# Performance work log

Measured on AMD Instinct MI355X. Metric: run time of the kernel, lower is better.

Reference implementation:

```python
import jax, jax.numpy as jnp
import numpy as np

EPS = 1e-5  # torch BatchNorm default eps
B, C, T, NOUT, NCLS = 4096, 32, 512, 16, 4


def setup_inputs() -> dict:
    key = jax.random.key(0)
    ks = jax.random.split(key, 12)
    s = lambda k, shape: jax.random.normal(k, shape, jnp.float32) * 0.05
    return {
        "de": jax.random.normal(ks[0], (B, C, T), jnp.float32),
        "adj": jax.random.normal(ks[1], (B, C, C), jnp.float32),  # unused by forward (module recomputes corr)
        "dw_w": s(ks[2], (C, 1, 3)),      # depthwise Conv1d weight [C,1,3]
        "dw_b": s(ks[3], (C,)),
        "pw_w": s(ks[4], (C, C)),          # pointwise 1x1 conv [out,in]
        "pw_b": s(ks[5], (C,)),
        "bn1_g": jnp.ones((C,), jnp.float32),
        "bn1_b": jnp.zeros((C,), jnp.float32),
        "gc_w": s(ks[6], (T, NOUT)),       # GraphConvolution weight
        "fc_w": s(ks[7], (C * NOUT, C)),   # fc62 Linear(512,32)
        "fc_b": s(ks[8], (C,)),
        "bn2_g": jnp.ones((C,), jnp.float32),
        "bn2_b": jnp.zeros((C,), jnp.float32),
        "cls_w": s(ks[9], (C, NCLS)),      # fcclass Linear(32,4)
        "cls_b": s(ks[10], (NCLS,)),
    }


def reference(de, adj, dw_w, dw_b, pw_w, pw_b, bn1_g, bn1_b, gc_w,
              fc_w, fc_b, bn2_g, bn2_b, cls_w, cls_b):
    # --- SeparableConv2d (really 1d): depthwise k=3 -> pointwise 1x1 -> BN -> relu ---
    x = jax.lax.conv_general_dilated(
        de, dw_w, window_strides=(1,), padding=[(1, 1)],
        dimension_numbers=("NCH", "OIH", "NCH"),
        feature_group_count=de.shape[1]) + dw_b[None, :, None]
    x = jnp.einsum("oc,bct->bot", pw_w, x) + pw_b[None, :, None]
    m = x.mean((0, 2), keepdims=True)
    v = x.var((0, 2), keepdims=True)  # biased, as BN normalization uses
    x = (x - m) / jnp.sqrt(v + EPS) * bn1_g[None, :, None] + bn1_b[None, :, None]
    x = jax.nn.relu(x)                       # [B, C, T]

    # --- batched Pearson corrcoef over the time axis (vectorizes the per-sample loop) ---
    xt = x.transpose(0, 2, 1)                # [B, T, C]
    Tn = xt.shape[1]
    f = (Tn - 1) / Tn
    xc = xt - xt.mean(1, keepdims=True)
    num = jnp.einsum("btn,btm->bnm", xc, xc) / Tn   # biased covariance
    var = xt.var(1, ddof=1)                         # torch var default unbiased
    den = jnp.sqrt(var[:, :, None] * var[:, None, :]) * f
    cor = num / den                          # [B, C, C]

    # --- Chebyshev graph convolution (single K term, adj = cor) + relu ---
    g = jnp.einsum("bnm,bmt->bnt", cor, x)   # message passing over channel graph
    g = jax.nn.relu(jnp.einsum("bnt,to->bno", g, gc_w))  # [B, C, 16]

    # --- fc62: Linear -> BN1d -> (dropout: identity) -> sigmoid ---
    h = g.reshape(g.shape[0], -1) @ fc_w + fc_b          # [B, 32]
    m2 = h.mean(0)
    v2 = h.var(0)
    h = (h - m2) / jnp.sqrt(v2 + EPS) * bn2_g + bn2_b
    h = jax.nn.sigmoid(h)

    return h @ cls_w + cls_b                 # [B, 4]
```

## Files before the change

### kernel.cpp

```cpp
#include <hip/hip_runtime.h>
#include <math.h>

#define BB 4096
#define CC 32
#define TT 512
#define NOUTC 16
#define EPSF 1e-5f
#define XS 520


typedef __attribute__((ext_vector_type(16))) float f32x16;
typedef __attribute__((ext_vector_type(4)))  float f32x4;
typedef __attribute__((ext_vector_type(8)))  short short8;
typedef __attribute__((ext_vector_type(8)))  _Float16 half8;
typedef __attribute__((ext_vector_type(4)))  unsigned int u32x4;
typedef __attribute__((ext_vector_type(2)))  unsigned int u32x2;
typedef __attribute__((ext_vector_type(2)))  float vf2;
typedef __attribute__((ext_vector_type(4)))  float vf4;
typedef vf4 __attribute__((aligned(4))) vf4u;
typedef vf2 __attribute__((aligned(4))) vf2u;

__device__ __forceinline__ unsigned short f2b(float f) {
  unsigned int u = __builtin_bit_cast(unsigned int, f);
  return (unsigned short)((u + 0x7FFFu + ((u >> 16) & 1u)) >> 16);
}
__device__ __forceinline__ float blo(unsigned int u) {
  return __builtin_bit_cast(float, u << 16);
}
__device__ __forceinline__ float bhi(unsigned int u) {
  return __builtin_bit_cast(float, u & 0xFFFF0000u);
}
__device__ __forceinline__ unsigned int pk2(float a, float b) {
  return (unsigned int)f2b(a) | ((unsigned int)f2b(b) << 16);
}
__device__ __forceinline__ unsigned short h16(float f) {
  _Float16 h = (_Float16)f;
  return __builtin_bit_cast(unsigned short, h);
}
__device__ __forceinline__ unsigned int h2pk(float a, float b) {
  return (unsigned int)h16(a) | ((unsigned int)h16(b) << 16);
}

__device__ __forceinline__ void conv_cols(const float* __restrict__ deb,
    const float* __restrict__ dw, const float* __restrict__ db_,
    int tid, float* x1A, float* x1B) {
  int t0 = tid * 2;
  int off = (tid == 0) ? 0 : ((tid == 255) ? t0 - 2 : t0 - 1);
#pragma unroll
  for (int c = 0; c < CC; c++) {
    vf4u v = *reinterpret_cast<const vf4u*>(deb + c * TT + off);
    float vm1 = (tid == 0) ? 0.f : ((tid == 255) ? v.y : v.x);
    float v0  = (tid == 0) ? v.x : ((tid == 255) ? v.z : v.y);
    float vp1 = (tid == 0) ? v.y : ((tid == 255) ? v.w : v.z);
    float vp2 = (tid == 0) ? v.z : ((tid == 255) ? 0.f : v.w);
    float w0 = dw[c * 3], w1 = dw[c * 3 + 1], w2 = dw[c * 3 + 2], bc = db_[c];
    x1A[c] = fmaf(w0, vm1, fmaf(w1, v0, fmaf(w2, vp1, bc)));
    x1B[c] = fmaf(w0, v0, fmaf(w1, vp1, fmaf(w2, vp2, bc)));
  }
}

__global__ __launch_bounds__(256, 4) void k1_stats(const float* __restrict__ de,
    const float* __restrict__ dw, const float* __restrict__ db_,
    const float* __restrict__ pw, const float* __restrict__ pwb,
    const float* __restrict__ gcw,
    float* __restrict__ wsv, unsigned short* __restrict__ gcf,
    unsigned int* __restrict__ x2h, int useWs) {
  __shared__ __align__(16) unsigned short ldsX[13392];
  __shared__ float pbe_s[CC];
  __shared__ float sqb[4][64];
  const int XFo = 0, A3o = 10320;

  int tid = threadIdx.x, b = blockIdx.x;
  int lane = tid & 63, w = tid >> 6;
  int m31 = lane & 31, kh = lane >> 5;
  int p = tid >> 7, rp = tid & 127;

  if (b == 0) {
    for (int i = tid; i < TT * NOUTC; i += 256) {
      int e = i & 7, ln = (i >> 3) & 63, j = (i >> 9) & 7, w2 = i >> 12;
      int q = ln >> 4, n16 = ln & 15;
      int t = w2 * 256 + q * 8 + j * 32 + e;
      gcf[i] = f2b(gcw[t * 16 + n16]);
    }
  }

  for (int i = tid; i < 3 * CC * CC; i += 256) {
    int k = i >> 10, rem = i & 1023, o = rem >> 5, c = rem & 31;
    ldsX[A3o + i] = h16(pw[o * CC + c] * dw[c * 3 + k]);
  }
  if (tid < CC) {
    float s = pwb[tid];
#pragma unroll
    for (int c = 0; c < CC; c++) s = fmaf(pw[tid * CC + c], db_[c], s);
    pbe_s[tid] = s;
  }

  const float* deb = de + (size_t)b * CC * TT;
  unsigned int* xw = x2h + (size_t)b * (CC * 256);

  float sA[16], qA[16];
#pragma unroll
  for (int r = 0; r < 16; r++) { sA[r] = 0.f; qA[r] = 0.f; }
  float pbv[16];

#pragma unroll
  for (int h = 0; h < 2; h++) {
    if (h > 0) __syncthreads();
    {
      int t0 = h * 256 + 2 * rp - 1;
      int r0 = 2 * rp;
      int tl = (t0 < 0) ? 0 : t0;
#pragma unroll
      for (int cc = 0; cc < 16; cc += 2) {
        int c = 16 * p + cc;
        vf2 va = *(const vf2u*)(deb + c * TT + tl);
        vf2 vb = *(const vf2u*)(deb + (c + 1) * TT + tl);
        if (t0 < 0) { va.y = va.x; va.x = 0.f; vb.y = vb.x; vb.x = 0.f; }
        *(unsigned int*)&ldsX[XFo + r0 * 40 + c] = h2pk(va.x, vb.x);
        *(unsigned int*)&ldsX[XFo + (r0 + 1) * 40 + c] = h2pk(va.y, vb.y);
      }
      if (rp >= 126) {
        int r2 = 256 + (rp - 126);
        int t2 = h * 256 + r2 - 1;
#pragma unroll
        for (int cc = 0; cc < 16; cc++) {
          int c = 16 * p + cc;
          float v = (t2 < TT) ? deb[c * TT + t2] : 0.f;
          ldsX[XFo + r2 * 40 + c] = h16(v);
        }
      }
    }
    __syncthreads();
    if (h == 0) {
#pragma unroll
      for (int r = 0; r < 16; r++) pbv[r] = pbe_s[(r & 3) + 8 * (r >> 2) + 4 * kh];
    }
#pragma unroll
    for (int i = 0; i < 2; i++) {
      int wt = w * 2 + i;
      f32x16 acc;
#pragma unroll
      for (int r = 0; r < 16; r++) acc[r] = 0.f;
      int rowb = wt * 32 + m31;
#pragma unroll
      for (int k = 0; k < 3; k++) {
#pragma unroll
        for (int s = 0; s < 2; s++) {
          half8 af = *(const half8*)&ldsX[A3o + k * 1024 + m31 * 32 + s * 16 + kh * 8];
          half8 bf = *(const half8*)&ldsX[XFo + (rowb + k) * 40 + s * 16 + kh * 8];
          acc = __builtin_amdgcn_mfma_f32_32x32x16_f16(af, bf, acc, 0, 0, 0);
        }
      }
#pragma unroll
      for (int q4 = 0; q4 < 4; q4++) {
        float v0 = acc[4 * q4 + 0] + pbv[4 * q4 + 0];
        float v1 = acc[4 * q4 + 1] + pbv[4 * q4 + 1];
        float v2 = acc[4 * q4 + 2] + pbv[4 * q4 + 2];
        float v3 = acc[4 * q4 + 3] + pbv[4 * q4 + 3];
        sA[4 * q4 + 0] += v0; qA[4 * q4 + 0] = fmaf(v0, v0, qA[4 * q4 + 0]);
        sA[4 * q4 + 1] += v1; qA[4 * q4 + 1] = fmaf(v1, v1, qA[4 * q4 + 1]);
        sA[4 * q4 + 2] += v2; qA[4 * q4 + 2] = fmaf(v2, v2, qA[4 * q4 + 2]);
        sA[4 * q4 + 3] += v3; qA[4 * q4 + 3] = fmaf(v3, v3, qA[4 * q4 + 3]);
        if (useWs) {
          u32x2 pr2;
          pr2[0] = pk2(v0, v1);
          pr2[1] = pk2(v2, v3);
          *(u32x2*)(xw + ((((size_t)h * 8 + wt) * 4 + q4) * 2 + kh) * 64 + m31 * 2) = pr2;
        }
      }
    }
  }

#pragma unroll
  for (int r = 0; r < 16; r++) {
    float s = sA[r], q = qA[r];
#pragma unroll
    for (int d = 1; d < 32; d <<= 1) { s += __shfl_xor(s, d); q += __shfl_xor(q, d); }
    sA[r] = s; qA[r] = q;
  }
  if (m31 == 0) {
#pragma unroll
    for (int r = 0; r < 16; r++) {
      int o = (r & 3) + 8 * (r >> 2) + 4 * kh;
      sqb[w][o * 2 + 0] = sA[r];
      sqb[w][o * 2 + 1] = qA[r];
    }
  }
  __syncthreads();
  if (tid < 64) {
    int o = tid >> 1, st = tid & 1;
    float v = sqb[0][tid] + sqb[1][tid] + sqb[2][tid] + sqb[3][tid];
    atomicAdd(&wsv[st * 32 + o], v);
  }
}

__global__ __launch_bounds__(256, 3) void k3_main(const float* __restrict__ de,
    const float* __restrict__ dw, const float* __restrict__ db_,
    const float* __restrict__ pw, const float* __restrict__ pwb,
    const float* __restrict__ wsv, const float* __restrict__ bn1g,
    const float* __restrict__ bn1b, const unsigned short* __restrict__ gcf,
    const float* __restrict__ fcw, const float* __restrict__ fcb,
    float* __restrict__ hT, const unsigned int* __restrict__ x2h, int useWs) {
  __shared__ __align__(16) unsigned short x_s[CC * XS];
  __shared__ float gramP[2][CC * CC];
  __shared__ float zP[2][CC * NOUTC];
  __shared__ float red16[CC * 8];
  __shared__ float mu_s[CC], inv_s[CC];
  __shared__ float scsh[64];

  int tid = threadIdx.x, b = blockIdx.x;
  int w = tid >> 6, lane = tid & 63;
  int t0 = tid * 2;

  if (tid < CC) {
    float N = (float)BB * (float)TT;
    float mean = wsv[tid] / N;
    float var = wsv[32 + tid] / N - mean * mean;
    float sc = bn1g[tid] / sqrtf(var + EPSF);
    scsh[tid] = sc;
    scsh[32 + tid] = bn1b[tid] - mean * sc;
  }
  __syncthreads();

  if (useWs) {
    const unsigned int* xr = x2h + (size_t)b * (CC * 256);
#pragma unroll
    for (int it = 0; it < 16; it++) {
      int g = it * 256 + tid;
      int m31g = g & 31, khg = (g >> 5) & 1, q4g = (g >> 6) & 3;
      int wtg = (g >> 8) & 7, hg = (g >> 11) & 1;
      u32x2 v = *(const u32x2*)(xr + (size_t)g * 2);
      int ob = 8 * q4g + 4 * khg;
      int t = hg * 256 + wtg * 32 + m31g;
      float f0 = fmaxf(fmaf(blo(v[0]), scsh[ob + 0], scsh[32 + ob + 0]), 0.f);
      float f1 = fmaxf(fmaf(bhi(v[0]), scsh[ob + 1], scsh[32 + ob + 1]), 0.f);
      float f2 = fmaxf(fmaf(blo(v[1]), scsh[ob + 2], scsh[32 + ob + 2]), 0.f);
      float f3 = fmaxf(fmaf(bhi(v[1]), scsh[ob + 3], scsh[32 + ob + 3]), 0.f);
      x_s[(ob + 0) * XS + t] = f2b(f0);
      x_s[(ob + 1) * XS + t] = f2b(f1);
      x_s[(ob + 2) * XS + t] = f2b(f2);
      x_s[(ob + 3) * XS + t] = f2b(f3);
    }
  } else {
    const float* deb = de + (size_t)b * CC * TT;
    float x1A[CC], x1B[CC];
    conv_cols(deb, dw, db_, tid, x1A, x1B);
#pragma unroll
    for (int o = 0; o < CC; o++) {
      float aA = pwb[o], aB = pwb[o];
#pragma unroll
      for (int c = 0; c < CC; c++) { float pv = pw[o * CC + c]; aA = fmaf(pv, x1A[c], aA); aB = fmaf(pv, x1B[c], aB); }
      float sc = scsh[o], sh = scsh[32 + o];
      unsigned short hA = f2b(fmaxf(fmaf(aA, sc, sh), 0.f));
      unsigned short hB = f2b(fmaxf(fmaf(aB, sc, sh), 0.f));
      *(unsigned int*)(&x_s[o * XS + t0]) = (unsigned int)hA | ((unsigned int)hB << 16);
    }
  }
  __syncthreads();

  {
    int c = tid >> 3, j = tid & 7;
    float s = 0.f;
#pragma unroll
    for (int it = 0; it < 8; it++) {
      u32x4 u = *reinterpret_cast<const u32x4*>(&x_s[c * XS + j * 64 + it * 8]);
#pragma unroll
      for (int k = 0; k < 4; k++) s += blo(u[k]) + bhi(u[k]);
    }
    red16[c * 8 + j] = s;
  }

  if (w < 2) {
    int m = lane & 31, kh = lane >> 5;
    f32x16 acc;
#pragma unroll
    for (int r = 0; r < 16; r++) acc[r] = 0.f;
    int kbase = w * 256 + kh * 8;
#pragma unroll
    for (int kk = 0; kk < 256; kk += 16) {
      short8 a = *(const short8*)(&x_s[m * XS + kbase + kk]);
      acc = __builtin_amdgcn_mfma_f32_32x32x16_bf16(a, a, acc, 0, 0, 0);
    }
#pragma unroll
    for (int r = 0; r < 16; r++) {
      int row = (r & 3) + 8 * (r >> 2) + 4 * kh;
      gramP[w][row * CC + m] = acc[r];
    }
  } else {
    int w2 = w - 2;
    int n16 = lane & 15, q = lane >> 4;
    f32x4 ac0, ac1;
#pragma unroll
    for (int r = 0; r < 4; r++) { ac0[r] = 0.f; ac1[r] = 0.f; }
    const unsigned short* gf = gcf + w2 * 4096;
    short8 bfr[8];
#pragma unroll
    for (int j = 0; j < 8; j++) bfr[j] = *(const short8*)(gf + (j * 64 + lane) * 8);
    int kbase = w2 * 256 + q * 8;
#pragma unroll
    for (int j = 0; j < 8; j++) {
      int kk = j * 32;
      short8 af0 = *(const short8*)(&x_s[n16 * XS + kbase + kk]);
      short8 af1 = *(const short8*)(&x_s[(16 + n16) * XS + kbase + kk]);
      ac0 = __builtin_amdgcn_mfma_f32_16x16x32_bf16(af0, bfr[j], ac0, 0, 0, 0);
      ac1 = __builtin_amdgcn_mfma_f32_16x16x32_bf16(af1, bfr[j], ac1, 0, 0, 0);
    }
#pragma unroll
    for (int r = 0; r < 4; r++) {
      int row = q * 4 + r;
      zP[w2][row * NOUTC + n16] = ac0[r];
      zP[w2][(16 + row) * NOUTC + n16] = ac1[r];
    }
  }
  __syncthreads();
  if (tid < CC) {
    float s = 0.f;
#pragma unroll
    for (int j = 0; j < 8; j++) s += red16[tid * 8 + j];
    mu_s[tid] = s;
  }
  __syncthreads();
  float* gram0 = gramP[0];
  float* Zi = zP[0];
  float* g2 = zP[1];
  for (int i = tid; i < CC * CC; i += 256) {
    int n = i >> 5, m = i & 31;
    gram0[i] = gram0[i] + gramP[1][i] - mu_s[n] * mu_s[m] * (1.f / (float)TT);
  }
  for (int i = tid; i < CC * NOUTC; i += 256) Zi[i] = zP[0][i] + zP[1][i];
  __syncthreads();
  if (tid < CC) inv_s[tid] = rsqrtf(gram0[tid * 32 + tid]);
  __syncthreads();
  for (int i = tid; i < CC * NOUTC; i += 256) {
    int n = i >> 4, o = i & 15;
    float s = 0.f;
#pragma unroll
    for (int m = 0; m < CC; m++) s = fmaf(gram0[n * 32 + m] * inv_s[m], Zi[m * NOUTC + o], s);
    g2[i] = fmaxf(s * inv_s[n], 0.f);
  }
  __syncthreads();
  float* red2 = gramP[1];
  {
    int j = tid & 31, ch = tid >> 5;
    float pacc = 0.f;
#pragma unroll
    for (int ii = 0; ii < 64; ii++) {
      int i = ch * 64 + ii;
      pacc = fmaf(g2[i], fcw[i * CC + j], pacc);
    }
    red2[j * 9 + ch] = pacc;
  }
  __syncthreads();
  if (tid < CC) {
    float h = fcb[tid];
#pragma unroll
    for (int ch = 0; ch < 8; ch++) h += red2[tid * 9 + ch];
    hT[(size_t)tid * BB + b] = h;
  }
}

__global__ void k4_bn2(const float* __restrict__ hT, const float* __restrict__ g,
                       const float* __restrict__ bta, float* __restrict__ ws) {
  __shared__ float redS[256], redQ[256];
  int j = blockIdx.x, tid = threadIdx.x;
  const float* row = hT + (size_t)j * BB;
  float s = 0, q = 0;
  for (int i = tid; i < BB; i += 256) { float v = row[i]; s += v; q = fmaf(v, v, q); }
  redS[tid] = s; redQ[tid] = q;
  __syncthreads();
  for (int k = 128; k > 0; k >>= 1) {
    if (tid < k) { redS[tid] += redS[tid + k]; redQ[tid] += redQ[tid + k]; }
    __syncthreads();
  }
  if (tid == 0) {
    float N = (float)BB;
    float mean = redS[0] / N;
    float var = redQ[0] / N - mean * mean;
    float sc = g[j] / sqrtf(var + EPSF);
    ws[64 + j] = sc;
    ws[96 + j] = bta[j] - mean * sc;
  }
}

__global__ void k5_out(const float* __restrict__ hT, const float* __restrict__ ws,
                       const float* __restrict__ clsw, const float* __restrict__ clsb,
                       float* __restrict__ out) {
  __shared__ float hs[CC * 257];
  int b0 = blockIdx.x * 256, tid = threadIdx.x;
  for (int i = tid; i < CC * 256; i += 256) {
    int j = i >> 8, bb = i & 255;
    float v = fmaf(hT[(size_t)j * BB + b0 + bb], ws[64 + j], ws[96 + j]);
    hs[j * 257 + bb] = 1.f / (1.f + expf(-v));
  }
  __syncthreads();
  float o0 = clsb[0], o1 = clsb[1], o2 = clsb[2], o3 = clsb[3];
#pragma unroll
  for (int j = 0; j < CC; j++) {
    float h = hs[j * 257 + tid];
    o0 = fmaf(h, clsw[j * 4 + 0], o0);
    o1 = fmaf(h, clsw[j * 4 + 1], o1);
    o2 = fmaf(h, clsw[j * 4 + 2], o2);
    o3 = fmaf(h, clsw[j * 4 + 3], o3);
  }
  float4* out4 = reinterpret_cast<float4*>(out);
  out4[b0 + tid] = make_float4(o0, o1, o2, o3);
}

extern "C" void kernel_launch(void* const* d_in, const int* in_sizes, int n_in,
                              void* d_out, int out_size, void* d_ws, size_t ws_size,
                              hipStream_t stream) {
  const float* de   = (const float*)d_in[0];
  const float* dw   = (const float*)d_in[2];
  const float* db_  = (const float*)d_in[3];
  const float* pw   = (const float*)d_in[4];
  const float* pwb  = (const float*)d_in[5];
  const float* bn1g = (const float*)d_in[6];
  const float* bn1b = (const float*)d_in[7];
  const float* gcw  = (const float*)d_in[8];
  const float* fcw  = (const float*)d_in[9];
  const float* fcb  = (const float*)d_in[10];
  const float* bn2g = (const float*)d_in[11];
  const float* bn2b = (const float*)d_in[12];
  const float* clsw = (const float*)d_in[13];
  const float* clsb = (const float*)d_in[14];

  float* ws = (float*)d_ws;
  unsigned short* gcf = (unsigned short*)(ws + 128);
  float* hT   = ws + 4224;
  unsigned int* x2h = (unsigned int*)(ws + 397440);
  float* out  = (float*)d_out;

  size_t need = ((size_t)397440 + 33554432ull) * 4ull;
  int useWs = (ws_size >= need) ? 1 : 0;

  hipMemsetAsync(d_ws, 0, 256, stream);
  k1_stats<<<BB, 256, 0, stream>>>(de, dw, db_, pw, pwb, gcw, ws, gcf, x2h, useWs);
  k3_main<<<BB, 256, 0, stream>>>(de, dw, db_, pw, pwb, ws, bn1g, bn1b, gcf, fcw, fcb, hT, x2h, useWs);
  k4_bn2<<<CC, 256, 0, stream>>>(hT, bn2g, bn2b, ws);
  k5_out<<<BB / 256, 256, 0, stream>>>(hT, ws, clsw, clsb, out);
}
```

Measured before the change: 524.7 us.

## Replace BN1 atomics with per-block partials and a reduce kernel; keep weights in registers

k1 now writes its per-block BN1 sums and sums of squares to a partials array instead of issuing global atomicAdds. A new k2_bn1 kernel reduces the partials, computes the BN1 scale and shift once, and also takes over the gc weight conversion that block 0 used to do. The fused depthwise/pointwise A-fragments are now built directly in registers rather than staged through LDS, which shrinks k1's shared memory. This removes atomic contention, the memset and the per-block BN finalisation, at the cost of one extra kernel launch and higher register pressure in k1.

```diff
diff --git a/kernel.cpp b/kernel.cpp
--- a/kernel.cpp
+++ b/kernel.cpp
@@ -62,31 +62,26 @@
 __global__ __launch_bounds__(256, 4) void k1_stats(const float* __restrict__ de,
     const float* __restrict__ dw, const float* __restrict__ db_,
     const float* __restrict__ pw, const float* __restrict__ pwb,
-    const float* __restrict__ gcw,
-    float* __restrict__ wsv, unsigned short* __restrict__ gcf,
-    unsigned int* __restrict__ x2h, int useWs) {
-  __shared__ __align__(16) unsigned short ldsX[13392];
+    float* __restrict__ part, unsigned int* __restrict__ x2h, int useWs) {
+  __shared__ __align__(16) unsigned short ldsX[258 * 40];
   __shared__ float pbe_s[CC];
   __shared__ float sqb[4][64];
-  const int XFo = 0, A3o = 10320;
 
   int tid = threadIdx.x, b = blockIdx.x;
   int lane = tid & 63, w = tid >> 6;
   int m31 = lane & 31, kh = lane >> 5;
   int p = tid >> 7, rp = tid & 127;
 
-  if (b == 0) {
-    for (int i = tid; i < TT * NOUTC; i += 256) {
-      int e = i & 7, ln = (i >> 3) & 63, j = (i >> 9) & 7, w2 = i >> 12;
-      int q = ln >> 4, n16 = ln & 15;
-      int t = w2 * 256 + q * 8 + j * 32 + e;
-      gcf[i] = f2b(gcw[t * 16 + n16]);
-    }
-  }
-
-  for (int i = tid; i < 3 * CC * CC; i += 256) {
-    int k = i >> 10, rem = i & 1023, o = rem >> 5, c = rem & 31;
-    ldsX[A3o + i] = h16(pw[o * CC + c] * dw[c * 3 + k]);
+  half8 af[3][2];
+#pragma unroll
+  for (int s = 0; s < 2; s++) {
+#pragma unroll
+    for (int j = 0; j < 8; j++) {
+      int c = s * 16 + kh * 8 + j;
+      float pv = pw[m31 * CC + c];
+#pragma unroll
+      for (int k = 0; k < 3; k++) af[k][s][j] = (_Float16)(pv * dw[c * 3 + k]);
+    }
   }
   if (tid < CC) {
     float s = pwb[tid];
@@ -101,7 +96,6 @@
   float sA[16], qA[16];
 #pragma unroll
   for (int r = 0; r < 16; r++) { sA[r] = 0.f; qA[r] = 0.f; }
-  float pbv[16];
 
 #pragma unroll
   for (int h = 0; h < 2; h++) {
@@ -116,8 +110,8 @@
         vf2 va = *(const vf2u*)(deb + c * TT + tl);
         vf2 vb = *(const vf2u*)(deb + (c + 1) * TT + tl);
         if (t0 < 0) { va.y = va.x; va.x = 0.f; vb.y = vb.x; vb.x = 0.f; }
-        *(unsigned int*)&ldsX[XFo + r0 * 40 + c] = h2pk(va.x, vb.x);
-        *(unsigned int*)&ldsX[XFo + (r0 + 1) * 40 + c] = h2pk(va.y, vb.y);
+        *(unsigned int*)&ldsX[r0 * 40 + c] = h2pk(va.x, vb.x);
+        *(unsigned int*)&ldsX[(r0 + 1) * 40 + c] = h2pk(va.y, vb.y);
       }
       if (rp >= 126) {
         int r2 = 256 + (rp - 126);
@@ -126,15 +120,12 @@
         for (int cc = 0; cc < 16; cc++) {
           int c = 16 * p + cc;
           float v = (t2 < TT) ? deb[c * TT + t2] : 0.f;
-          ldsX[XFo + r2 * 40 + c] = h16(v);
+          ldsX[r2 * 40 + c] = h16(v);
         }
       }
     }
     __syncthreads();
-    if (h == 0) {
-#pragma unroll
-      for (int r = 0; r < 16; r++) pbv[r] = pbe_s[(r & 3) + 8 * (r >> 2) + 4 * kh];
-    }
+
 #pragma unroll
     for (int i = 0; i < 2; i++) {
       int wt = w * 2 + i;
@@ -146,17 +137,17 @@
       for (int k = 0; k < 3; k++) {
 #pragma unroll
         for (int s = 0; s < 2; s++) {
-          half8 af = *(const half8*)&ldsX[A3o + k * 1024 + m31 * 32 + s * 16 + kh * 8];
-          half8 bf = *(const half8*)&ldsX[XFo + (rowb + k) * 40 + s * 16 + kh * 8];
-          acc = __builtin_amdgcn_mfma_f32_32x32x16_f16(af, bf, acc, 0, 0, 0);
+          half8 bf = *(const half8*)&ldsX[(rowb + k) * 40 + s * 16 + kh * 8];
+          acc = __builtin_amdgcn_mfma_f32_32x32x16_f16(af[k][s], bf, acc, 0, 0, 0);
         }
       }
 #pragma unroll
       for (int q4 = 0; q4 < 4; q4++) {
-        float v0 = acc[4 * q4 + 0] + pbv[4 * q4 + 0];
-        float v1 = acc[4 * q4 + 1] + pbv[4 * q4 + 1];
-        float v2 = acc[4 * q4 + 2] + pbv[4 * q4 + 2];
-        float v3 = acc[4 * q4 + 3] + pbv[4 * q4 + 3];
+        int ob = 8 * q4 + 4 * kh;
+        float v0 = acc[4 * q4 + 0] + pbe_s[ob + 0];
+        float v1 = acc[4 * q4 + 1] + pbe_s[ob + 1];
+        float v2 = acc[4 * q4 + 2] + pbe_s[ob + 2];
+        float v3 = acc[4 * q4 + 3] + pbe_s[ob + 3];
         sA[4 * q4 + 0] += v0; qA[4 * q4 + 0] = fmaf(v0, v0, qA[4 * q4 + 0]);
         sA[4 * q4 + 1] += v1; qA[4 * q4 + 1] = fmaf(v1, v1, qA[4 * q4 + 1]);
         sA[4 * q4 + 2] += v2; qA[4 * q4 + 2] = fmaf(v2, v2, qA[4 * q4 + 2]);
@@ -190,15 +181,46 @@
   if (tid < 64) {
     int o = tid >> 1, st = tid & 1;
     float v = sqb[0][tid] + sqb[1][tid] + sqb[2][tid] + sqb[3][tid];
-    atomicAdd(&wsv[st * 32 + o], v);
+    part[(size_t)(st * 32 + o) * BB + b] = v;
+  }
+}
+
+__global__ void k2_bn1(const float* __restrict__ part, const float* __restrict__ g,
+                       const float* __restrict__ bta, float* __restrict__ ws,
+                       const float* __restrict__ gcw, unsigned short* __restrict__ gcf) {
+  __shared__ float redS[256], redQ[256];
+  int o = blockIdx.x, tid = threadIdx.x;
+  {
+    int i = o * 256 + tid;
+    int e = i & 7, ln = (i >> 3) & 63, j = (i >> 9) & 7, w2 = i >> 12;
+    int q = ln >> 4, n16 = ln & 15;
+    int t = w2 * 256 + q * 8 + j * 32 + e;
+    gcf[i] = f2b(gcw[t * 16 + n16]);
+  }
+  const float* ps = part + (size_t)o * BB;
+  const float* pq = part + (size_t)(CC + o) * BB;
+  float s = 0, q = 0;
+  for (int i = tid; i < BB; i += 256) { s += ps[i]; q += pq[i]; }
+  redS[tid] = s; redQ[tid] = q;
+  __syncthreads();
+  for (int k = 128; k > 0; k >>= 1) {
+    if (tid < k) { redS[tid] += redS[tid + k]; redQ[tid] += redQ[tid + k]; }
+    __syncthreads();
+  }
+  if (tid == 0) {
+    float N = (float)BB * (float)TT;
+    float mean = redS[0] / N;
+    float var = redQ[0] / N - mean * mean;
+    float sc = g[o] / sqrtf(var + EPSF);
+    ws[o] = sc;
+    ws[32 + o] = bta[o] - mean * sc;
   }
 }
 
 __global__ __launch_bounds__(256, 3) void k3_main(const float* __restrict__ de,
     const float* __restrict__ dw, const float* __restrict__ db_,
     const float* __restrict__ pw, const float* __restrict__ pwb,
-    const float* __restrict__ wsv, const float* __restrict__ bn1g,
-    const float* __restrict__ bn1b, const unsigned short* __restrict__ gcf,
+    const float* __restrict__ wsv, const unsigned short* __restrict__ gcf,
     const float* __restrict__ fcw, const float* __restrict__ fcb,
     float* __restrict__ hT, const unsigned int* __restrict__ x2h, int useWs) {
   __shared__ __align__(16) unsigned short x_s[CC * XS];
@@ -212,14 +234,7 @@
   int w = tid >> 6, lane = tid & 63;
   int t0 = tid * 2;
 
-  if (tid < CC) {
-    float N = (float)BB * (float)TT;
-    float mean = wsv[tid] / N;
-    float var = wsv[32 + tid] / N - mean * mean;
-    float sc = bn1g[tid] / sqrtf(var + EPSF);
-    scsh[tid] = sc;
-    scsh[32 + tid] = bn1b[tid] - mean * sc;
-  }
+  if (tid < 64) scsh[tid] = wsv[tid];
   __syncthreads();
 
   if (useWs) {
@@ -427,15 +442,16 @@
   float* ws = (float*)d_ws;
   unsigned short* gcf = (unsigned short*)(ws + 128);
   float* hT   = ws + 4224;
+  float* part = ws + 135296;
   unsigned int* x2h = (unsigned int*)(ws + 397440);
   float* out  = (float*)d_out;
 
   size_t need = ((size_t)397440 + 33554432ull) * 4ull;
   int useWs = (ws_size >= need) ? 1 : 0;
 
-  hipMemsetAsync(d_ws, 0, 256, stream);
-  k1_stats<<<BB, 256, 0, stream>>>(de, dw, db_, pw, pwb, gcw, ws, gcf, x2h, useWs);
-  k3_main<<<BB, 256, 0, stream>>>(de, dw, db_, pw, pwb, ws, bn1g, bn1b, gcf, fcw, fcb, hT, x2h, useWs);
+  k1_stats<<<BB, 256, 0, stream>>>(de, dw, db_, pw, pwb, part, x2h, useWs);
+  k2_bn1<<<CC, 256, 0, stream>>>(part, bn1g, bn1b, ws, gcw, gcf);
+  k3_main<<<BB, 256, 0, stream>>>(de, dw, db_, pw, pwb, ws, gcf, fcw, fcb, hT, x2h, useWs);
   k4_bn2<<<CC, 256, 0, stream>>>(hT, bn2g, bn2b, ws);
   k5_out<<<BB / 256, 256, 0, stream>>>(hT, ws, clsw, clsb, out);
 }
```

Measured after the change: 493.4 us. -6.0%, faster.
